# Performance work log

Hardware: AMD Instinct MI355X
Metric: run time of the kernel (lower is better)

The kernel has to match this reference:

```python
import jax, jax.numpy as jnp
import numpy as np

Q = 16293   # quantization_channels
R = 24      # residual_channels
D = 32      # dilation_channels
S = 128     # skip_channels
K = 2       # filter_width
NL = 8      # number of residual blocks
B = 4       # batch_size
L = 2048    # input sequence length
RECEPTIVE = (K - 1) * sum([1, 2, 4, 8, 16, 32, 64, 128]) + K  # 257
OUT_W = L - RECEPTIVE + 1  # 1792


def setup_inputs() -> dict:
    key = jax.random.key(0)
    ks = jax.random.split(key, 9)
    sc = 0.05
    return {
        "idx": jax.random.randint(ks[0], (B, L), 0, Q, dtype=jnp.int32),
        "pre_W": jax.random.normal(ks[1], (K, Q, R), jnp.float32) * sc,
        "filt_W": jax.random.normal(ks[2], (NL, K, R, D), jnp.float32) * sc,
        "gate_W": jax.random.normal(ks[3], (NL, K, R, D), jnp.float32) * sc,
        "res_W": jax.random.normal(ks[4], (NL, D, R), jnp.float32) * sc,
        "skip_W": jax.random.normal(ks[5], (NL, D, S), jnp.float32) * sc,
        "post_W1": jax.random.normal(ks[6], (S, S), jnp.float32) * sc,
        "post_W2": jax.random.normal(ks[7], (S, Q), jnp.float32) * sc,
    }


def _conv2(x, W):
    # kernel_size=2, dilation=1 (the original passes dilations[0]=1 to every
    # block), 'valid' padding: out[t] = x[t] @ W[0] + x[t+1] @ W[1]
    return jnp.einsum('btc,cf->btf', x[:, :-1], W[0]) + \
           jnp.einsum('btc,cf->btf', x[:, 1:], W[1])


def reference(idx, pre_W, filt_W, gate_W, res_W, skip_W, post_W1, post_W2):
    # one_hot(idx, Q) followed by a width-2 conv == two-tap embedding gather
    x = pre_W[0][idx[:, :-1]] + pre_W[1][idx[:, 1:]]  # [B, L-1, R]
    skip_sum = jnp.zeros((B, OUT_W, S), x.dtype)
    for i in range(NL):
        out = jnp.tanh(_conv2(x, filt_W[i])) * jax.nn.sigmoid(_conv2(x, gate_W[i]))
        # training-mode slice: skip_cut = T_out - output_width
        out_skip = out[:, -OUT_W:]                                  # [B, OUT_W, D]
        skip_sum = skip_sum + jnp.einsum('btd,ds->bts', out_skip, skip_W[i])
        transformed = jnp.einsum('btd,dr->btr', out, res_W[i])      # [B, T-1, R]
        x = x[:, 1:] + transformed                                  # residual, cut input
    h = jax.nn.relu(skip_sum)
    h = jax.nn.relu(jnp.einsum('bts,su->btu', h, post_W1))
    logits = jnp.einsum('bts,sq->btq', h, post_W2)                  # [B, OUT_W, Q]
    return logits
```

## Files before the change

### kernel.cpp

```cpp
#include <hip/hip_runtime.h>
#include <stdint.h>

#define BB 4
#define LL 2048
#define QQ 16293
#define RR 24
#define DD 32
#define SS 128
#define NLAYER 8
#define OUTW 1792
#define TT0 2047
#define MROWS (BB*OUTW)
#define NPAD 16384
#define WCH 28

typedef float v4f __attribute__((ext_vector_type(4)));
typedef short v8s __attribute__((ext_vector_type(8)));

static __device__ __forceinline__ unsigned short f2bf(float x) {
  unsigned int u = __float_as_uint(x);
  unsigned int r = (u + 0x7fffu + ((u >> 16) & 1u)) >> 16;
  return (unsigned short)r;
}

static __device__ __forceinline__ float fast_sigmoid(float z) {
  return __builtin_amdgcn_rcpf(1.0f + __expf(-z));
}
static __device__ __forceinline__ float fast_tanh(float z) {
  return 1.0f - 2.0f * __builtin_amdgcn_rcpf(1.0f + __expf(2.0f * z));
}

__global__ __launch_bounds__(1024) void fused_layers_kernel(
    const int* __restrict__ idx, const float* __restrict__ preW,
    const float* __restrict__ filtW, const float* __restrict__ gateW,
    const float* __restrict__ resW, const float* __restrict__ skipW,
    float* __restrict__ skip_out) {
  int b = blockIdx.y;
  int j0 = blockIdx.x * WCH;
  int lane = (int)(threadIdx.x & 63);
  int w = __builtin_amdgcn_readfirstlane((int)(threadIdx.x >> 6));

  __shared__ float x_t[2][RR][66];
  __shared__ float out_s[64][33];

  for (int z = (int)threadIdx.x; z < 2 * RR * 2; z += 1024) {
    int bu = z & 1;
    int cc = 64 + ((z >> 1) & 1);
    int r = z >> 2;
    x_t[bu][r][cc] = 0.f;
  }

  int tbase = j0 + 247;
  if (w < 12) {
    int t = tbase + lane;
    if (t > TT0 - 1) t = TT0 - 1;
    int i0 = idx[b * LL + t];
    int i1 = idx[b * LL + t + 1];
    const float* p0 = preW + (size_t)i0 * RR + 2 * w;
    const float* p1 = preW + (size_t)QQ * RR + (size_t)i1 * RR + 2 * w;
#pragma unroll
    for (int rr = 0; rr < 2; ++rr)
      x_t[0][2 * w + rr][lane] = p0[rr] + p1[rr];
  }

  float sk[8];
#pragma unroll
  for (int c = 0; c < 8; ++c) sk[c] = 0.f;

  __syncthreads();

  for (int i = 0; i < NLAYER; ++i) {
    int cur = i & 1, nxt = cur ^ 1;
    int lmax = 62 - i;

    float xa[RR], xb[RR];
#pragma unroll
    for (int r = 0; r < RR; ++r) {
      xa[r] = x_t[cur][r][lane];
      xb[r] = x_t[cur][r][lane + 1];
    }
    const float* Fw = filtW + (size_t)i * 2 * RR * DD;
    const float* Gw = gateW + (size_t)i * 2 * RR * DD;
    float zf[2], zg[2];
#pragma unroll
    for (int dd = 0; dd < 2; ++dd) { zf[dd] = 0.f; zg[dd] = 0.f; }
#pragma unroll
    for (int r = 0; r < RR; ++r) {
#pragma unroll
      for (int dd = 0; dd < 2; ++dd) {
        int d = w * 2 + dd;
        zf[dd] = fmaf(xa[r], Fw[r * DD + d], zf[dd]);
        zf[dd] = fmaf(xb[r], Fw[RR * DD + r * DD + d], zf[dd]);
        zg[dd] = fmaf(xa[r], Gw[r * DD + d], zg[dd]);
        zg[dd] = fmaf(xb[r], Gw[RR * DD + r * DD + d], zg[dd]);
      }
    }
    if (lane <= lmax) {
#pragma unroll
      for (int dd = 0; dd < 2; ++dd)
        out_s[lane][w * 2 + dd] = fast_tanh(zf[dd]) * fast_sigmoid(zg[dd]);
    }
    __syncthreads();

    if (lane < WCH) {
      const float* Sw = skipW + (size_t)i * DD * SS + w * 8;
#pragma unroll
      for (int d = 0; d < DD; ++d) {
        float o = out_s[lane + 7 - i][d];
#pragma unroll
        for (int c = 0; c < 8; ++c)
          sk[c] = fmaf(o, Sw[d * SS + c], sk[c]);
      }
    }

    if (w < 12 && lane <= lmax) {
      const float* Rw = resW + (size_t)i * DD * RR;
#pragma unroll
      for (int rr = 0; rr < 2; ++rr) {
        int r = w * 2 + rr;
        float acc = x_t[cur][r][lane + 1];
#pragma unroll
        for (int d = 0; d < DD; ++d)
          acc = fmaf(out_s[lane][d], Rw[d * RR + r], acc);
        x_t[nxt][r][lane] = acc;
      }
    }
    __syncthreads();
  }

  if (lane < WCH) {
    float* sp = skip_out + ((size_t)b * OUTW + j0 + lane) * SS + w * 8;
#pragma unroll
    for (int c4 = 0; c4 < 2; ++c4) {
      float4 v;
      v.x = sk[4 * c4 + 0]; v.y = sk[4 * c4 + 1];
      v.z = sk[4 * c4 + 2]; v.w = sk[4 * c4 + 3];
      *(float4*)(sp + 4 * c4) = v;
    }
  }
}

__global__ __launch_bounds__(256) void h1_kernel(const float* __restrict__ skip_sum,
                                                 const float* __restrict__ W1,
                                                 unsigned short* __restrict__ h1) {
  int m0 = blockIdx.x * 32;
  int tc = threadIdx.x & 31;
  int tr = threadIdx.x >> 5;
  __shared__ float h_s[32][128];
#pragma unroll
  for (int it = 0; it < 16; ++it) {
    int lin = it * 256 + (int)threadIdx.x;
    int rrow = lin >> 7, d = lin & 127;
    float v = skip_sum[(size_t)(m0 + rrow) * SS + d];
    h_s[rrow][d] = v > 0.f ? v : 0.f;
  }
  __syncthreads();

  float acc[4][4];
#pragma unroll
  for (int rr = 0; rr < 4; ++rr)
#pragma unroll
    for (int c = 0; c < 4; ++c) acc[rr][c] = 0.f;

#pragma unroll 4
  for (int d = 0; d < 128; ++d) {
    float4 wv = *(const float4*)(W1 + (size_t)d * SS + tc * 4);
#pragma unroll
    for (int rr = 0; rr < 4; ++rr) {
      float hv = h_s[tr * 4 + rr][d];
      acc[rr][0] = fmaf(hv, wv.x, acc[rr][0]);
      acc[rr][1] = fmaf(hv, wv.y, acc[rr][1]);
      acc[rr][2] = fmaf(hv, wv.z, acc[rr][2]);
      acc[rr][3] = fmaf(hv, wv.w, acc[rr][3]);
    }
  }
#pragma unroll
  for (int rr = 0; rr < 4; ++rr) {
    int row = m0 + tr * 4 + rr;
    ushort4 u;
    u.x = f2bf(fmaxf(acc[rr][0], 0.f));
    u.y = f2bf(fmaxf(acc[rr][1], 0.f));
    u.z = f2bf(fmaxf(acc[rr][2], 0.f));
    u.w = f2bf(fmaxf(acc[rr][3], 0.f));
    *(ushort4*)(h1 + (size_t)row * SS + tc * 4) = u;
  }
}

__global__ __launch_bounds__(256) void w2t_kernel(const float* __restrict__ W2,
                                                  unsigned short* __restrict__ W2T) {
  int n0 = blockIdx.x * 64;
  __shared__ float t_s[64][129];
#pragma unroll
  for (int it = 0; it < 32; ++it) {
    int lin = it * 256 + (int)threadIdx.x;
    int k = lin >> 6, nn = lin & 63;
    int n = n0 + nn;
    t_s[nn][k] = (n < QQ) ? W2[(size_t)k * QQ + n] : 0.f;
  }
  __syncthreads();
#pragma unroll
  for (int it = 0; it < 4; ++it) {
    int lin = it * 256 + (int)threadIdx.x;
    int nn = lin >> 4, slot = lin & 15;
    v8s val;
#pragma unroll
    for (int jj = 0; jj < 8; ++jj) val[jj] = (short)f2bf(t_s[nn][slot * 8 + jj]);
    *(v8s*)(W2T + ((size_t)(n0 + nn)) * 128 + slot * 8) = val;
  }
}

struct GemmLds {
  union {
    struct { unsigned short A_s[128 * 128]; unsigned short B_s[128 * 128]; } ab;
    float c_s[128][132];
  };
};

__global__ __launch_bounds__(256) void gemm_kernel(const unsigned short* __restrict__ A,
                                                   const unsigned short* __restrict__ Bm,
                                                   float* __restrict__ Cc) {
  __shared__ GemmLds sh;
  unsigned short* A_s = sh.ab.A_s;
  unsigned short* B_s = sh.ab.B_s;
  int m0 = blockIdx.y * 128;
  int n0 = blockIdx.x * 128;
  int tid = threadIdx.x;

#pragma unroll
  for (int it = 0; it < 8; ++it) {
    int lin = it * 256 + tid;
    int row = lin >> 4, slot = lin & 15;
    int sw = slot ^ (row & 7);
    uint4 va = *(const uint4*)(A + ((size_t)(m0 + row)) * 128 + slot * 8);
    *(uint4*)(A_s + row * 128 + sw * 8) = va;
    uint4 vb = *(const uint4*)(Bm + ((size_t)(n0 + row)) * 128 + slot * 8);
    *(uint4*)(B_s + row * 128 + sw * 8) = vb;
  }
  __syncthreads();

  int lane = tid & 63;
  int w = tid >> 6;
  int wm = (w >> 1) * 64, wn = (w & 1) * 64;
  int lr = lane & 15, g = lane >> 4;

  v4f acc[4][4];
#pragma unroll
  for (int mf = 0; mf < 4; ++mf)
#pragma unroll
    for (int nf = 0; nf < 4; ++nf) {
      v4f z = {0.f, 0.f, 0.f, 0.f};
      acc[mf][nf] = z;
    }

#pragma unroll
  for (int ks = 0; ks < 4; ++ks) {
    int kg = ks * 4 + g;
    v8s a[4], bfr[4];
#pragma unroll
    for (int mf = 0; mf < 4; ++mf) {
      int row = wm + mf * 16 + lr;
      a[mf] = *(v8s*)(A_s + row * 128 + ((kg ^ (row & 7)) * 8));
    }
#pragma unroll
    for (int nf = 0; nf < 4; ++nf) {
      int row = wn + nf * 16 + lr;
      bfr[nf] = *(v8s*)(B_s + row * 128 + ((kg ^ (row & 7)) * 8));
    }
#pragma unroll
    for (int mf = 0; mf < 4; ++mf)
#pragma unroll
      for (int nf = 0; nf < 4; ++nf)
        acc[mf][nf] = __builtin_amdgcn_mfma_f32_16x16x32_bf16(a[mf], bfr[nf], acc[mf][nf], 0, 0, 0);
  }

  __syncthreads();
#pragma unroll
  for (int mf = 0; mf < 4; ++mf)
#pragma unroll
    for (int reg = 0; reg < 4; ++reg) {
      int row = wm + mf * 16 + g * 4 + reg;
#pragma unroll
      for (int nf = 0; nf < 4; ++nf)
        sh.c_s[row][wn + nf * 16 + lr] = acc[mf][nf][reg];
    }
  __syncthreads();

  int slot = tid & 31;
  int rsub = tid >> 5;
  bool edge = (n0 + 128 > QQ);
#pragma unroll
  for (int it = 0; it < 16; ++it) {
    int row = it * 8 + rsub;
    int n = n0 + slot * 4;
    v4f v = *(v4f*)(&sh.c_s[row][slot * 4]);
    float* crow = Cc + (size_t)(m0 + row) * QQ;
    if (!edge) {
      __builtin_nontemporal_store(v, (v4f*)(crow + n));
    } else {
      if (n + 3 < QQ) {
        __builtin_nontemporal_store(v, (v4f*)(crow + n));
      } else {
        if (n + 0 < QQ) crow[n + 0] = v.x;
        if (n + 1 < QQ) crow[n + 1] = v.y;
        if (n + 2 < QQ) crow[n + 2] = v.z;
        if (n + 3 < QQ) crow[n + 3] = v.w;
      }
    }
  }
}

extern "C" void kernel_launch(void* const* d_in, const int* in_sizes, int n_in,
                              void* d_out, int out_size, void* d_ws, size_t ws_size,
                              hipStream_t stream) {
  (void)in_sizes; (void)n_in; (void)out_size; (void)ws_size;
  const int*   idx   = (const int*)d_in[0];
  const float* preW  = (const float*)d_in[1];
  const float* filtW = (const float*)d_in[2];
  const float* gateW = (const float*)d_in[3];
  const float* resW  = (const float*)d_in[4];
  const float* skipW = (const float*)d_in[5];
  const float* W1    = (const float*)d_in[6];
  const float* W2    = (const float*)d_in[7];
  float* out = (float*)d_out;

  char* ws = (char*)d_ws;
  float* skip = (float*)(ws);
  unsigned short* h1  = (unsigned short*)(ws + 3670016);
  unsigned short* W2T = (unsigned short*)(ws + 5505024);

  w2t_kernel<<<dim3(NPAD / 64), 256, 0, stream>>>(W2, W2T);
  fused_layers_kernel<<<dim3(OUTW / WCH, BB), 1024, 0, stream>>>(idx, preW, filtW, gateW,
                                                                 resW, skipW, skip);
  h1_kernel<<<dim3(MROWS / 32), 256, 0, stream>>>(skip, W1, h1);
  gemm_kernel<<<dim3(NPAD / 128, MROWS / 128), 256, 0, stream>>>(h1, W2T, out);
}
```

Before: 272.7 us.

## Keep A fragments in registers across N tiles and align output stores

The output GEMM now loads each block's A fragments straight from global memory into registers once, then loops over eight N tiles. The B fragments are read directly from global memory with no LDS staging. Stores are realigned per row so float4 writes land on 16-byte aligned addresses, because the row stride QQ is odd; the nontemporal hints are dropped. The aim is to cut redundant A loads and misaligned stores on this store-bound kernel, at the cost of fewer blocks and uncoalesced direct B fragment loads.

Measured after the change: 400.2 us. +46.7%, slower.

```diff
diff --git a/kernel.cpp b/kernel.cpp
--- a/kernel.cpp
+++ b/kernel.cpp
@@ -13,6 +13,7 @@
 #define MROWS (BB*OUTW)
 #define NPAD 16384
 #define WCH 28
+#define NTILE 8
 
 typedef float v4f __attribute__((ext_vector_type(4)));
 typedef short v8s __attribute__((ext_vector_type(8)));
@@ -209,101 +210,97 @@
   }
 }
 
-struct GemmLds {
-  union {
-    struct { unsigned short A_s[128 * 128]; unsigned short B_s[128 * 128]; } ab;
-    float c_s[128][132];
-  };
-};
-
 __global__ __launch_bounds__(256) void gemm_kernel(const unsigned short* __restrict__ A,
                                                    const unsigned short* __restrict__ Bm,
                                                    float* __restrict__ Cc) {
-  __shared__ GemmLds sh;
-  unsigned short* A_s = sh.ab.A_s;
-  unsigned short* B_s = sh.ab.B_s;
+  __shared__ float c_s[128][132];
   int m0 = blockIdx.y * 128;
-  int n0 = blockIdx.x * 128;
+  int n0 = blockIdx.x * (128 * NTILE);
   int tid = threadIdx.x;
-
-#pragma unroll
-  for (int it = 0; it < 8; ++it) {
-    int lin = it * 256 + tid;
-    int row = lin >> 4, slot = lin & 15;
-    int sw = slot ^ (row & 7);
-    uint4 va = *(const uint4*)(A + ((size_t)(m0 + row)) * 128 + slot * 8);
-    *(uint4*)(A_s + row * 128 + sw * 8) = va;
-    uint4 vb = *(const uint4*)(Bm + ((size_t)(n0 + row)) * 128 + slot * 8);
-    *(uint4*)(B_s + row * 128 + sw * 8) = vb;
-  }
-  __syncthreads();
-
   int lane = tid & 63;
   int w = tid >> 6;
   int wm = (w >> 1) * 64, wn = (w & 1) * 64;
   int lr = lane & 15, g = lane >> 4;
 
-  v4f acc[4][4];
+  v8s afr[4][4];
 #pragma unroll
   for (int mf = 0; mf < 4; ++mf)
 #pragma unroll
-    for (int nf = 0; nf < 4; ++nf) {
-      v4f z = {0.f, 0.f, 0.f, 0.f};
-      acc[mf][nf] = z;
-    }
-
-#pragma unroll
-  for (int ks = 0; ks < 4; ++ks) {
-    int kg = ks * 4 + g;
-    v8s a[4], bfr[4];
-#pragma unroll
-    for (int mf = 0; mf < 4; ++mf) {
-      int row = wm + mf * 16 + lr;
-      a[mf] = *(v8s*)(A_s + row * 128 + ((kg ^ (row & 7)) * 8));
-    }
-#pragma unroll
-    for (int nf = 0; nf < 4; ++nf) {
-      int row = wn + nf * 16 + lr;
-      bfr[nf] = *(v8s*)(B_s + row * 128 + ((kg ^ (row & 7)) * 8));
-    }
-#pragma unroll
-    for (int mf = 0; mf < 4; ++mf)
-#pragma unroll
-      for (int nf = 0; nf < 4; ++nf)
-        acc[mf][nf] = __builtin_amdgcn_mfma_f32_16x16x32_bf16(a[mf], bfr[nf], acc[mf][nf], 0, 0, 0);
-  }
-
-  __syncthreads();
-#pragma unroll
-  for (int mf = 0; mf < 4; ++mf)
-#pragma unroll
-    for (int reg = 0; reg < 4; ++reg) {
-      int row = wm + mf * 16 + g * 4 + reg;
-#pragma unroll
-      for (int nf = 0; nf < 4; ++nf)
-        sh.c_s[row][wn + nf * 16 + lr] = acc[mf][nf][reg];
-    }
-  __syncthreads();
+    for (int ks = 0; ks < 4; ++ks)
+      afr[mf][ks] = *(const v8s*)(A + ((size_t)(m0 + wm + mf * 16 + lr)) * 128 + (ks * 4 + g) * 8);
 
   int slot = tid & 31;
   int rsub = tid >> 5;
-  bool edge = (n0 + 128 > QQ);
-#pragma unroll
-  for (int it = 0; it < 16; ++it) {
-    int row = it * 8 + rsub;
-    int n = n0 + slot * 4;
-    v4f v = *(v4f*)(&sh.c_s[row][slot * 4]);
-    float* crow = Cc + (size_t)(m0 + row) * QQ;
-    if (!edge) {
-      __builtin_nontemporal_store(v, (v4f*)(crow + n));
-    } else {
-      if (n + 3 < QQ) {
-        __builtin_nontemporal_store(v, (v4f*)(crow + n));
+  int am = rsub & 3;
+  int a0 = (4 - am) & 3;
+
+#pragma unroll 1
+  for (int j = 0; j < NTILE; ++j) {
+    int nb = n0 + j * 128;
+
+    v4f acc[4][4];
+#pragma unroll
+    for (int mf = 0; mf < 4; ++mf)
+#pragma unroll
+      for (int nf = 0; nf < 4; ++nf) {
+        v4f z = {0.f, 0.f, 0.f, 0.f};
+        acc[mf][nf] = z;
+      }
+
+#pragma unroll
+    for (int ks = 0; ks < 4; ++ks) {
+      v8s bfr[4];
+#pragma unroll
+      for (int nf = 0; nf < 4; ++nf)
+        bfr[nf] = *(const v8s*)(Bm + ((size_t)(nb + wn + nf * 16 + lr)) * 128 + (ks * 4 + g) * 8);
+#pragma unroll
+      for (int mf = 0; mf < 4; ++mf)
+#pragma unroll
+        for (int nf = 0; nf < 4; ++nf)
+          acc[mf][nf] = __builtin_amdgcn_mfma_f32_16x16x32_bf16(afr[mf][ks], bfr[nf], acc[mf][nf], 0, 0, 0);
+    }
+
+    __syncthreads();
+#pragma unroll
+    for (int mf = 0; mf < 4; ++mf)
+#pragma unroll
+      for (int reg = 0; reg < 4; ++reg) {
+        int row = wm + mf * 16 + g * 4 + reg;
+#pragma unroll
+        for (int nf = 0; nf < 4; ++nf)
+          c_s[row][wn + nf * 16 + lr] = acc[mf][nf][reg];
+      }
+    __syncthreads();
+
+    bool edge = (nb + 128 > QQ);
+#pragma unroll
+    for (int it = 0; it < 16; ++it) {
+      int row = it * 8 + rsub;
+      float* crow = Cc + (size_t)(m0 + row) * QQ;
+      if (slot < 31) {
+        int off = a0 + 4 * slot;
+        int n = nb + off;
+        v4f v;
+        v[0] = c_s[row][off + 0];
+        v[1] = c_s[row][off + 1];
+        v[2] = c_s[row][off + 2];
+        v[3] = c_s[row][off + 3];
+        if (!edge) {
+          *(v4f*)(crow + n) = v;
+        } else if (n + 3 < QQ) {
+          *(v4f*)(crow + n) = v;
+        } else {
+#pragma unroll
+          for (int e = 0; e < 4; ++e)
+            if (n + e < QQ) crow[n + e] = v[e];
+        }
       } else {
-        if (n + 0 < QQ) crow[n + 0] = v.x;
-        if (n + 1 < QQ) crow[n + 1] = v.y;
-        if (n + 2 < QQ) crow[n + 2] = v.z;
-        if (n + 3 < QQ) crow[n + 3] = v.w;
+#pragma unroll
+        for (int e = 0; e < 4; ++e) {
+          int col = (e < 4 - a0) ? (a0 + 124 + e) : (e - (4 - a0));
+          int n = nb + col;
+          if (!edge || n < QQ) crow[n] = c_s[row][col];
+        }
       }
     }
   }
@@ -332,5 +329,5 @@
   fused_layers_kernel<<<dim3(OUTW / WCH, BB), 1024, 0, stream>>>(idx, preW, filtW, gateW,
                                                                  resW, skipW, skip);
   h1_kernel<<<dim3(MROWS / 32), 256, 0, stream>>>(skip, W1, h1);
-  gemm_kernel<<<dim3(NPAD / 128, MROWS / 128), 256, 0, stream>>>(h1, W2T, out);
-}
+  gemm_kernel<<<dim3(NPAD / (128 * NTILE), MROWS / 128), 256, 0, stream>>>(h1, W2T, out);
+}
```
